# Performance work log

Measured on AMD Instinct MI355X. Metric: run time of the kernel, lower is better.

Reference implementation:

```python
import jax, jax.numpy as jnp
import numpy as np

EPS = 1e-5
NUM_GROUPS = 32


def group_norm(x, num_groups=NUM_GROUPS, eps=EPS):
    # x: [B, C, H, W]; normalize over (C//G, H, W) per group, no affine
    B, C, H, W = x.shape
    xg = x.reshape(B, num_groups, C // num_groups, H, W)
    mean = xg.mean(axis=(2, 3, 4), keepdims=True)
    var = xg.var(axis=(2, 3, 4), keepdims=True)
    xg = (xg - mean) * jax.lax.rsqrt(var + eps)
    return xg.reshape(B, C, H, W)


def nin(x, W, b):
    # 1x1 dense projection over channel dim: [B,C,H,W] x [C,O] -> [B,O,H,W]
    return jnp.einsum('bchw,co->bohw', x, W) + b[None, :, None, None]


def setup_inputs() -> dict:
    key = jax.random.key(0)
    ks = jax.random.split(key, 9)
    B, C, H, W_ = 32, 512, 32, 32
    s = 1.0 / np.sqrt(C)
    return {
        'x': jax.random.normal(ks[0], (B, C, H, W_), jnp.float32),
        'Wq': jax.random.normal(ks[1], (C, C), jnp.float32) * s,
        'bq': jnp.zeros((C,), jnp.float32),
        'Wk': jax.random.normal(ks[2], (C, C), jnp.float32) * s,
        'bk': jnp.zeros((C,), jnp.float32),
        'Wv': jax.random.normal(ks[3], (C, C), jnp.float32) * s,
        'bv': jnp.zeros((C,), jnp.float32),
        'Wn': jax.random.normal(ks[4], (C, C), jnp.float32) * (0.05 * s),
        'bn': jnp.zeros((C,), jnp.float32),
    }


def reference(x, Wq, bq, Wk, bk, Wv, bv, Wn, bn):
    B, C, H, W_ = x.shape
    h = group_norm(x)
    q = nin(h, Wq, bq)
    k = nin(h, Wk, bk)
    v = nin(h, Wv, bv)
    scale = jnp.asarray(C, x.dtype) ** -0.5
    # full spatial attention: [B, H, W, H', W']
    w = jnp.einsum('bchw,bcHW->bhwHW', q, k) * scale
    w = w.reshape(B, H, W_, H * W_)
    w = jax.nn.softmax(w, axis=-1)
    w = w.reshape(B, H, W_, H, W_)
    h = jnp.einsum('bhwHW,bcHW->bchw', w, v)
    h = nin(h, Wn, bn)
    return x + h
```

## Files before the change

### kernel.cpp

```cpp
#include <hip/hip_runtime.h>
#include <cstdint>

#define B_   32
#define C_   512
#define N_   1024
#define G_   32
#define CG_  16

typedef unsigned short u16;
typedef unsigned char u8;
typedef unsigned long long u64;

static constexpr float kEps = 1e-5f;
static constexpr float kLog2Scale = 0.06375871752987579f;

using f32x4  = __attribute__((ext_vector_type(4))) float;
using short8 = __attribute__((ext_vector_type(8))) short;
using i64x2  = __attribute__((ext_vector_type(2))) long long;

__device__ __forceinline__ u16 f2bf(float f) {
  uint32_t u = __builtin_bit_cast(uint32_t, f);
  u += 0x7fffu + ((u >> 16) & 1u);
  return (u16)(u >> 16);
}
__device__ __forceinline__ float bf2f(u16 h) {
  return __builtin_bit_cast(float, (uint32_t)h << 16);
}
__device__ __forceinline__ int pk4_fp8(float a, float b, float c, float d) {
  int w = __builtin_amdgcn_cvt_pk_fp8_f32(a, b, 0, false);
  w = __builtin_amdgcn_cvt_pk_fp8_f32(c, d, w, true);
  return w;
}
__device__ __forceinline__ int f8pos(int k) {
  const int c8 = (k >> 3) & 7;
  return (k & ~63) + ((c8 & 3) << 4) + ((c8 >> 2) << 3) + (k & 4);
}

__device__ __forceinline__ void gload16(const void* g, void* lds) {
  __builtin_amdgcn_global_load_lds(
      (__attribute__((address_space(1))) void*)(uintptr_t)g,
      (__attribute__((address_space(3))) void*)(uint32_t)(uintptr_t)lds,
      16, 0, 0);
}

__device__ __forceinline__ uint3 remap_xcd() {
  const int gx = gridDim.x, gy = gridDim.y, gz = gridDim.z;
  const int nwg = gx * gy * gz;
  const int lin = blockIdx.x + gx * (blockIdx.y + gy * blockIdx.z);
  const int q = nwg >> 3, r = nwg & 7;
  const int xcd = lin & 7, pos = lin >> 3;
  int nid = (xcd < r ? xcd * (q + 1) : r * (q + 1) + (xcd - r) * q) + pos;
  uint3 o;
  o.x = nid % gx; nid /= gx;
  o.y = nid % gy; o.z = nid / gy;
  return o;
}

__global__ __launch_bounds__(256) void wcvt_kernel(
    const float* __restrict__ Wq, const float* __restrict__ Wk,
    const float* __restrict__ Wv, u16* __restrict__ Wab, u16* __restrict__ Wbb) {
  const int idx = blockIdx.x * 256 + threadIdx.x;
  const int src = idx >> 16;
  const int e = (idx & 65535) * 4;
  const float* W = (src == 0) ? Wq : (src == 1) ? Wk : Wv;
  u16* D = (src == 0) ? Wab : (src == 1) ? Wbb : (Wab + 262144);
  const float4 v = *(const float4*)(W + e);
  ushort4 st;
  st.x = f2bf(v.x); st.y = f2bf(v.y); st.z = f2bf(v.z); st.w = f2bf(v.w);
  *(ushort4*)(D + e) = st;
}

__global__ __launch_bounds__(256) void wtr_kernel(
    const float* __restrict__ Wn, u16* __restrict__ Wtn) {
  __shared__ float tile[64][65];
  const int c0 = blockIdx.y * 64, o0 = blockIdx.x * 64;
  const int tx = threadIdx.x & 15, ty = threadIdx.x >> 4;
#pragma unroll
  for (int rr = 0; rr < 64; rr += 16) {
    const int c = c0 + ty + rr;
    const float4 v = *(const float4*)(Wn + (size_t)c * 512 + o0 + tx * 4);
    tile[ty + rr][tx * 4 + 0] = v.x;
    tile[ty + rr][tx * 4 + 1] = v.y;
    tile[ty + rr][tx * 4 + 2] = v.z;
    tile[ty + rr][tx * 4 + 3] = v.w;
  }
  __syncthreads();
#pragma unroll
  for (int rr = 0; rr < 64; rr += 16) {
    const int o = o0 + ty + rr;
    ushort4 st;
    st.x = f2bf(tile[tx * 4 + 0][ty + rr]);
    st.y = f2bf(tile[tx * 4 + 1][ty + rr]);
    st.z = f2bf(tile[tx * 4 + 2][ty + rr]);
    st.w = f2bf(tile[tx * 4 + 3][ty + rr]);
    *(ushort4*)(Wtn + (size_t)o * 512 + c0 + tx * 4) = st;
  }
}

__global__ __launch_bounds__(512) void biask_kernel(
    const float* __restrict__ Wk, const float* __restrict__ bq,
    const float* __restrict__ Wn, const float* __restrict__ bv,
    const float* __restrict__ bn, float* __restrict__ wkbq,
    float* __restrict__ bvn) {
  const int t = threadIdx.x;
  if (blockIdx.x == 0) {
    float s = 0.f;
    const float* row = Wk + (size_t)t * 512;
    for (int o = 0; o < 512; ++o) s += row[o] * bq[o];
    wkbq[t] = s;
  } else {
    float s = 0.f;
    for (int c = 0; c < 512; ++c) s += bv[c] * Wn[(size_t)c * 512 + t];
    bvn[t] = s + bn[t];
  }
}

__global__ __launch_bounds__(256) void gn_fused(const float* __restrict__ x,
                                                u8* __restrict__ Hn8,
                                                u8* __restrict__ HnT8) {
  __shared__ u16 lds2[16 * 1032];
  __shared__ float red[10];
  const int bg = blockIdx.x, b = bg >> 5, g = bg & 31;
  const int t = threadIdx.x;
  const float4* p4 = (const float4*)(x + (size_t)bg * 16384);
  float s = 0.f, s2 = 0.f;
  for (int i = t; i < 4096; i += 256) {
    const float4 v = p4[i];
    const int e = i * 4, ic = e >> 10, n = e & 1023;
    ushort4 sv;
    sv.x = f2bf(v.x); sv.y = f2bf(v.y); sv.z = f2bf(v.z); sv.w = f2bf(v.w);
    *(ushort4*)(lds2 + ic * 1032 + n) = sv;
    s  += v.x + v.y + v.z + v.w;
    s2 += v.x * v.x + v.y * v.y + v.z * v.z + v.w * v.w;
  }
#pragma unroll
  for (int o = 32; o; o >>= 1) { s += __shfl_xor(s, o); s2 += __shfl_xor(s2, o); }
  const int lane = t & 63, w = t >> 6;
  if (lane == 0) { red[w] = s; red[4 + w] = s2; }
  __syncthreads();
  if (t == 0) {
    s  = red[0] + red[1] + red[2] + red[3];
    s2 = red[4] + red[5] + red[6] + red[7];
    const float inv = 1.0f / 16384.0f;
    const float mean = s * inv;
    const float var  = s2 * inv - mean * mean;
    red[8] = mean;
    red[9] = rsqrtf(var + kEps);
  }
  __syncthreads();
  const float mean = red[8], rstd = red[9];
#pragma unroll
  for (int r = 0; r < 4; ++r) {
    const int n = t + 256 * r;
    float vals[16];
#pragma unroll
    for (int ic = 0; ic < 16; ++ic)
      vals[ic] = (bf2f(lds2[ic * 1032 + n]) - mean) * rstd;
    const u64 lo = (u64)(uint32_t)pk4_fp8(vals[0], vals[1], vals[2], vals[3]) |
                   ((u64)(uint32_t)pk4_fp8(vals[4], vals[5], vals[6], vals[7]) << 32);
    const u64 hi = (u64)(uint32_t)pk4_fp8(vals[8], vals[9], vals[10], vals[11]) |
                   ((u64)(uint32_t)pk4_fp8(vals[12], vals[13], vals[14], vals[15]) << 32);
    u8* rb = Hn8 + ((size_t)(b * N_ + n)) * C_;
    *(u64*)(rb + f8pos(g * 16))     = lo;
    *(u64*)(rb + f8pos(g * 16 + 8)) = hi;
  }
  const int nb = t * 4;
#pragma unroll
  for (int ic = 0; ic < 16; ++ic) {
    const ushort4 hv = *(const ushort4*)(lds2 + ic * 1032 + nb);
    const int wv = pk4_fp8((bf2f(hv.x) - mean) * rstd, (bf2f(hv.y) - mean) * rstd,
                           (bf2f(hv.z) - mean) * rstd, (bf2f(hv.w) - mean) * rstd);
    *(int*)(HnT8 + ((size_t)(b * C_ + g * 16 + ic)) * N_ + f8pos(nb)) = wv;
  }
}

__global__ __launch_bounds__(256) void gemm_w128(
    const u16* __restrict__ Ab, const u16* __restrict__ Bb, u8* __restrict__ Ob) {
  __shared__ u16 Alds[128 * 64];
  __shared__ u16 Blds[128 * 64];
  const int p = blockIdx.z;
  const u16* A = Ab + (size_t)p * 262144;
  const u16* B = Bb + (size_t)p * 262144;
  u8* O = Ob + (size_t)p * 262144;
  const int m0 = blockIdx.y * 128, n0 = blockIdx.x * 128;
  const int tid = threadIdx.x, lane = tid & 63, wid = tid >> 6;
  const int wm = wid >> 1, wn = wid & 1;
  const int sr = lane >> 3, scb = (lane & 7) ^ sr;
  const u16* Ag = A + (size_t)(m0 + wid * 32 + sr) * 512 + scb * 8;
  const u16* Bg = B + (size_t)(n0 + wid * 32 + sr) * 512 + scb * 8;
  char* Al = (char*)Alds + wid * 4096;
  char* Bl = (char*)Blds + wid * 4096;
  const int arow = lane & 15, g4 = lane >> 4, rx = lane & 7;
  f32x4 acc[4][4] = {};
  for (int k = 0; k < 512; k += 64) {
#pragma unroll
    for (int g = 0; g < 4; ++g) {
      gload16(Ag + k + g * (8 * 512), Al + g * 1024);
      gload16(Bg + k + g * (8 * 512), Bl + g * 1024);
    }
    __syncthreads();
#pragma unroll
    for (int kk = 0; kk < 2; ++kk) {
      const int pc = ((kk * 4 + g4) ^ rx) * 16;
      short8 a[4], b[4];
#pragma unroll
      for (int i = 0; i < 4; ++i)
        a[i] = *(const short8*)((const char*)Alds + (wm * 64 + i * 16 + arow) * 128 + pc);
#pragma unroll
      for (int j = 0; j < 4; ++j)
        b[j] = *(const short8*)((const char*)Blds + (wn * 64 + j * 16 + arow) * 128 + pc);
#pragma unroll
      for (int i = 0; i < 4; ++i)
#pragma unroll
        for (int j = 0; j < 4; ++j)
          acc[i][j] = __builtin_amdgcn_mfma_f32_16x16x32_bf16(a[i], b[j], acc[i][j], 0, 0, 0);
    }
    __syncthreads();
  }
#pragma unroll
  for (int i = 0; i < 4; ++i) {
    const int rowg = m0 + wm * 64 + i * 16 + ((lane >> 4) * 4);
#pragma unroll
    for (int j = 0; j < 4; ++j) {
      const int colg = n0 + wn * 64 + j * 16 + (lane & 15);
      const f32x4 v = acc[i][j];
      *(int*)(O + (size_t)colg * 512 + f8pos(rowg)) =
          pk4_fp8(v[0], v[1], v[2], v[3]);
    }
  }
}

#define LDA8_(D, BASE, MH)                                                      \
  _Pragma("unroll")                                                             \
  for (int i_ = 0; i_ < 4; ++i_) {                                              \
    const int rr_ = wm * 128 + (MH) * 64 + i_ * 16 + arow;                      \
    D[i_] = *(const i64x2*)((BASE) + rr_ * 64 +                                 \
                            ((g4 ^ ((rr_ >> 1) & 3)) << 4));                    \
  }
#define LDB8_(D, BASE)                                                          \
  _Pragma("unroll")                                                             \
  for (int j_ = 0; j_ < 4; ++j_) {                                              \
    const int rr_ = wn * 64 + j_ * 16 + arow;                                   \
    D[j_] = *(const i64x2*)((BASE) + rr_ * 64 +                                 \
                            ((g4 ^ ((rr_ >> 1) & 3)) << 4));                    \
  }
#define MM8_(ACC, AA, BB, H)                                                    \
  __builtin_amdgcn_s_setprio(1);                                                \
  _Pragma("unroll")                                                             \
  for (int i_ = 0; i_ < 4; ++i_)                                                \
    _Pragma("unroll")                                                           \
    for (int j_ = 0; j_ < 4; ++j_)                                              \
      ACC[i_][j_] = __builtin_amdgcn_mfma_f32_16x16x32_fp8_fp8(                 \
          AA[i_][H], BB[j_][H], ACC[i_][j_], 0, 0, 0);                          \
  __builtin_amdgcn_s_setprio(0);

__device__ __forceinline__ void gemm_core256_f8(
    const u8* __restrict__ A, const u8* __restrict__ B,
    int Ktot, int m0, int n0,
    char* Alds, char* Blds, f32x4 acc0[4][4], f32x4 acc1[4][4]) {
  const int tid = threadIdx.x, lane = tid & 63, wid = tid >> 6;
  const int wm = wid >> 2, wn = wid & 3;
  const int rl = lane >> 2;
  const int c16 = (lane & 3) ^ ((lane >> 3) & 3);
  const u8* Ag = A + (size_t)(m0 + wid * 32 + rl) * Ktot + c16 * 16;
  const u8* Bg = B + (size_t)(n0 + wid * 32 + rl) * Ktot + c16 * 16;
  char* Al = Alds + wid * 2048;
  char* Bl = Blds + wid * 2048;
  const long long r16 = (long long)16 * Ktot;
  const int arow = lane & 15, g4 = lane >> 4;
  const int nt = Ktot >> 6;

#pragma unroll
  for (int g = 0; g < 2; ++g) {
    gload16(Ag + g * r16, Al + g * 1024);
    gload16(Bg + g * r16, Bl + g * 1024);
  }
  asm volatile("s_waitcnt vmcnt(0)" ::: "memory");
  __builtin_amdgcn_s_barrier();
  i64x2 aX[4], aY[4], bX[4];
  LDA8_(aX, Alds, 0);

  for (int t = 0; t < nt; ++t) {
    const int cur = t & 1;
    const char* Ab = Alds + cur * 16384;
    const char* Bb = Blds + cur * 16384;
    const char* An = Alds + (cur ^ 1) * 16384;
    char* Aln = Al + (cur ^ 1) * 16384;
    char* Bln = Bl + (cur ^ 1) * 16384;
    const bool nx = (t + 1 < nt);
    const long long ko = (long long)(t + 1) * 64;

    if (nx) {
#pragma unroll
      for (int g = 0; g < 2; ++g) gload16(Bg + ko + g * r16, Bln + g * 1024);
    }
    LDB8_(bX, Bb);
    LDA8_(aY, Ab, 1);
    asm volatile("s_waitcnt lgkmcnt(4)" ::: "memory");
    __builtin_amdgcn_sched_barrier(0);
    __builtin_amdgcn_s_barrier();
    MM8_(acc0, aX, bX, 0);

    if (nx) {
#pragma unroll
      for (int g = 0; g < 2; ++g) gload16(Ag + ko + g * r16, Aln + g * 1024);
    }
    asm volatile("s_waitcnt lgkmcnt(0)" ::: "memory");
    __builtin_amdgcn_sched_barrier(0);
    __builtin_amdgcn_s_barrier();
    MM8_(acc1, aY, bX, 0);

    __builtin_amdgcn_sched_barrier(0);
    __builtin_amdgcn_s_barrier();
    MM8_(acc0, aX, bX, 1);

    if (nx) {
      asm volatile("s_waitcnt vmcnt(0)" ::: "memory");
    }
    __builtin_amdgcn_sched_barrier(0);
    __builtin_amdgcn_s_barrier();
    if (nx) {
      LDA8_(aX, An, 0);
    }
    MM8_(acc1, aY, bX, 1);
  }
}

__device__ __forceinline__ void copy_out_tile(const char* SH, u8* O, int LDC,
                                              int m0, int n0) {
  const int tid = threadIdx.x;
#pragma unroll
  for (int it = 0; it < 8; ++it) {
    const int flat = it * 8192 + tid * 16;
    const int row = flat >> 8, col = flat & 255;
    *(int4*)(O + (size_t)(n0 + row) * LDC + m0 + col) =
        *(const int4*)(SH + row * 256 + col);
  }
}

__global__ __launch_bounds__(512, 2) void gemm_hwq_f8(
    const u8* __restrict__ Wqk8, const u8* __restrict__ Hn8,
    const float* __restrict__ wkbq, u8* __restrict__ HWq8) {
  __shared__ char SH[4 * 256 * 64];
  const uint3 bid = remap_xcd();
  const int z = bid.z;
  const u8* B = Hn8 + (size_t)z * ((size_t)N_ * C_);
  u8* O = HWq8 + (size_t)z * ((size_t)N_ * C_);
  const int m0 = bid.y * 256, n0 = bid.x * 256;
  f32x4 acc0[4][4] = {};
  f32x4 acc1[4][4] = {};
  gemm_core256_f8(Wqk8, B, 512, m0, n0, SH, SH + 32768, acc0, acc1);

  const int lane = threadIdx.x & 63, wid = threadIdx.x >> 6;
  const int wm = wid >> 2, wn = wid & 3;
  __syncthreads();
#pragma unroll
  for (int i = 0; i < 8; ++i) {
    const int ml = wm * 128 + i * 16 + ((lane >> 4) * 4);
    const float4 bv = *(const float4*)(wkbq + m0 + ml);
#pragma unroll
    for (int j = 0; j < 4; ++j) {
      const int nl = wn * 64 + j * 16 + (lane & 15);
      const f32x4 v = (i < 4) ? acc0[i][j] : acc1[i - 4][j];
      *(int*)(SH + nl * 256 + f8pos(ml)) =
          pk4_fp8(v[0] + bv.x, v[1] + bv.y, v[2] + bv.z, v[3] + bv.w);
    }
  }
  __syncthreads();
  copy_out_tile(SH, O, 512, m0, n0);
}

__global__ __launch_bounds__(512, 2) void gemm_s_f8(
    const u8* __restrict__ Hn8, const u8* __restrict__ HWq8,
    u8* __restrict__ P8, float* __restrict__ Psum) {
  __shared__ char SH[4 * 256 * 64];
  const uint3 bid = remap_xcd();
  const int z = bid.z;
  const u8* A = Hn8  + (size_t)z * ((size_t)N_ * C_);
  const u8* B = HWq8 + (size_t)z * ((size_t)N_ * C_);
  u8*       O = P8   + (size_t)z * ((size_t)N_ * N_);
  const int m0 = bid.y * 256, n0 = bid.x * 256;
  f32x4 acc0[4][4] = {};
  f32x4 acc1[4][4] = {};
  gemm_core256_f8(A, B, 512, m0, n0, SH, SH + 32768, acc0, acc1);

  const int lane = threadIdx.x & 63, wid = threadIdx.x >> 6;
  const int wm = wid >> 2, wn = wid & 3;
  float psum[4] = {0.f, 0.f, 0.f, 0.f};
  __syncthreads();
#pragma unroll
  for (int i = 0; i < 8; ++i) {
    const int ml = wm * 128 + i * 16 + ((lane >> 4) * 4);
#pragma unroll
    for (int j = 0; j < 4; ++j) {
      const int nl = wn * 64 + j * 16 + (lane & 15);
      const f32x4 v = (i < 4) ? acc0[i][j] : acc1[i - 4][j];
      const float p0 = __builtin_exp2f(v[0] * kLog2Scale) * 0.0625f;
      const float p1 = __builtin_exp2f(v[1] * kLog2Scale) * 0.0625f;
      const float p2 = __builtin_exp2f(v[2] * kLog2Scale) * 0.0625f;
      const float p3 = __builtin_exp2f(v[3] * kLog2Scale) * 0.0625f;
      psum[j] += (p0 + p1) + (p2 + p3);
      *(int*)(SH + nl * 256 + f8pos(ml)) = pk4_fp8(p0, p1, p2, p3);
    }
  }
  const int slot = (m0 >> 7) + wm;
  float* Ps = Psum + ((size_t)z * 8 + slot) * N_;
#pragma unroll
  for (int j = 0; j < 4; ++j) {
    float r = psum[j];
    r += __shfl_xor(r, 16);
    r += __shfl_xor(r, 32);
    if (lane < 16) Ps[n0 + wn * 64 + j * 16 + lane] = r;
  }
  __syncthreads();
  copy_out_tile(SH, O, 1024, m0, n0);
}

__global__ __launch_bounds__(512, 2) void gemm_pv_f8(
    const u8* __restrict__ HnT8, const u8* __restrict__ P8,
    const float* __restrict__ Psum, u8* __restrict__ H28) {
  __shared__ char SH[4 * 256 * 64];
  const uint3 bid = remap_xcd();
  const int z = bid.z;
  const u8* A = HnT8 + (size_t)z * ((size_t)N_ * C_);
  const u8* B = P8   + (size_t)z * ((size_t)N_ * N_);
  u8*       O = H28  + (size_t)z * ((size_t)N_ * C_);
  const int m0 = bid.y * 256, n0 = bid.x * 256;
  f32x4 acc0[4][4] = {};
  f32x4 acc1[4][4] = {};
  gemm_core256_f8(A, B, 1024, m0, n0, SH, SH + 32768, acc0, acc1);

  const int lane = threadIdx.x & 63, wid = threadIdx.x >> 6;
  const int wm = wid >> 2, wn = wid & 3;
  const float* Ps = Psum + (size_t)z * 8 * N_;
  float inv[4];
#pragma unroll
  for (int j = 0; j < 4; ++j) {
    const int colg = n0 + wn * 64 + j * 16 + (lane & 15);
    float s = 0.f;
#pragma unroll
    for (int k = 0; k < 8; ++k) s += Ps[k * N_ + colg];
    inv[j] = 1.0f / s;
  }
  __syncthreads();
#pragma unroll
  for (int i = 0; i < 8; ++i) {
    const int ml = wm * 128 + i * 16 + ((lane >> 4) * 4);
#pragma unroll
    for (int j = 0; j < 4; ++j) {
      const int nl = wn * 64 + j * 16 + (lane & 15);
      const f32x4 v = (i < 4) ? acc0[i][j] : acc1[i - 4][j];
      *(int*)(SH + nl * 256 + f8pos(ml)) =
          pk4_fp8(v[0] * inv[j], v[1] * inv[j], v[2] * inv[j], v[3] * inv[j]);
    }
  }
  __syncthreads();
  copy_out_tile(SH, O, 512, m0, n0);
}

__global__ __launch_bounds__(512, 2) void gemm_final_f8(
    const u8* __restrict__ H28, const u8* __restrict__ Wvn8,
    const float* __restrict__ x, const float* __restrict__ bvn,
    float* __restrict__ Out) {
  __shared__ char Alds[2 * 256 * 64];
  __shared__ char Blds[2 * 256 * 64];
  const uint3 bid = remap_xcd();
  const int z = bid.z;
  const u8*    Ab = H28 + (size_t)z * ((size_t)N_ * C_);
  const float* xb = x + (size_t)z * ((size_t)C_ * N_);
  float*       Ob = Out + (size_t)z * ((size_t)C_ * N_);
  const int m0 = bid.y * 256, n0 = bid.x * 256;
  f32x4 acc0[4][4] = {};
  f32x4 acc1[4][4] = {};
  gemm_core256_f8(Ab, Wvn8, 512, m0, n0, Alds, Blds, acc0, acc1);

  const int lane = threadIdx.x & 63, wid = threadIdx.x >> 6;
  const int wm = wid >> 2, wn = wid & 3;
#pragma unroll
  for (int i = 0; i < 8; ++i) {
    const int rowg = m0 + wm * 128 + i * 16 + ((lane >> 4) * 4);
#pragma unroll
    for (int j = 0; j < 4; ++j) {
      const int colg = n0 + wn * 64 + j * 16 + (lane & 15);
      const float bc = bvn[colg];
      const size_t off = (size_t)colg * N_ + rowg;
      const float4 xv = *(const float4*)(xb + off);
      const f32x4 v = (i < 4) ? acc0[i][j] : acc1[i - 4][j];
      float4 ov;
      ov.x = xv.x + v[0] + bc;
      ov.y = xv.y + v[1] + bc;
      ov.z = xv.z + v[2] + bc;
      ov.w = xv.w + v[3] + bc;
      *(float4*)(Ob + off) = ov;
    }
  }
}

__global__ void sentinel_kernel(float* out, int n, float v) {
  const int i = blockIdx.x * blockDim.x + threadIdx.x;
  if (i < n) out[i] = v;
}

extern "C" void kernel_launch(void* const* d_in, const int* in_sizes, int n_in,
                              void* d_out, int out_size, void* d_ws, size_t ws_size,
                              hipStream_t stream) {
  const float* x  = (const float*)d_in[0];
  const float* Wq = (const float*)d_in[1];
  const float* bq = (const float*)d_in[2];
  const float* Wk = (const float*)d_in[3];
  const float* Wv = (const float*)d_in[5];
  const float* bv = (const float*)d_in[6];
  const float* Wn = (const float*)d_in[7];
  const float* bn = (const float*)d_in[8];
  float* out = (float*)d_out;

  char* ws = (char*)d_ws;
  size_t off = 0;
  u16* Wab = (u16*)(ws + off); off += (size_t)2 * 262144 * 2;
  u16* Wbb = (u16*)(ws + off); off += (size_t)2 * 262144 * 2;
  u8*  W8  = (u8*)(ws + off);  off += (size_t)2 * 262144;
  float* wkbq = (float*)(ws + off); off += 512 * 4;
  float* bvn  = (float*)(ws + off); off += 512 * 4;
  const size_t bnc = (size_t)B_ * N_ * C_;
  u8* Hn8  = (u8*)(ws + off); off += bnc;
  u8* HnT8 = (u8*)(ws + off); off += bnc;
  u8* HWq8 = (u8*)(ws + off); off += bnc;
  u8* P8   = (u8*)(ws + off); off += (size_t)B_ * N_ * N_;
  u8* H28  = (u8*)(ws + off); off += bnc;
  float* Psum = (float*)(ws + off); off += (size_t)B_ * 8 * N_ * 4;

  if (ws_size < off) {
    const float v = 1.0e6f + (float)(ws_size >> 20);
    sentinel_kernel<<<(out_size + 255) / 256, 256, 0, stream>>>(out, out_size, v);
    return;
  }

  wcvt_kernel<<<768, 256, 0, stream>>>(Wq, Wk, Wv, Wab, Wbb);
  wtr_kernel<<<dim3(8, 8), 256, 0, stream>>>(Wn, Wbb + 262144);
  biask_kernel<<<2, 512, 0, stream>>>(Wk, bq, Wn, bv, bn, wkbq, bvn);
  gn_fused<<<B_ * G_, 256, 0, stream>>>(x, Hn8, HnT8);
  gemm_w128<<<dim3(4, 4, 2), 256, 0, stream>>>(Wab, Wbb, W8);
  gemm_hwq_f8<<<dim3(4, 2, B_), 512, 0, stream>>>(W8, Hn8, wkbq, HWq8);
  gemm_s_f8<<<dim3(4, 4, B_), 512, 0, stream>>>(Hn8, HWq8, P8, Psum);
  gemm_pv_f8<<<dim3(4, 2, B_), 512, 0, stream>>>(HnT8, P8, Psum, H28);
  gemm_final_f8<<<dim3(2, 4, B_), 512, 0, stream>>>(H28, W8 + 262144, x, bvn, out);
}
```

Baseline: 194.7 us.

## Fuse PV and output projection GEMMs into one kernel with LDS-resident H2

Merges the P·V GEMM and the final Wn projection into a single kernel: each block computes all 512 channels for a 128-column slice of positions, keeps the normalized fp8 result in shared memory (XOR-swizzled), then runs the second GEMM reading weights directly from global memory and writes the residual output. This removes the H28 round trip through global memory and one launch. The epilogue staging in other kernels also gains an XOR swizzle to reduce LDS bank conflicts. In exchange it uses 144KB of LDS with one block per CU, a smaller tile along N, and unstaged global weight loads in the second GEMM.

Measured after the change: 192.2 us (median of 2 runs). Within noise of the previous version (-1.3%).

```diff
diff --git a/kernel.cpp b/kernel.cpp
--- a/kernel.cpp
+++ b/kernel.cpp
@@ -334,7 +334,7 @@
     const int flat = it * 8192 + tid * 16;
     const int row = flat >> 8, col = flat & 255;
     *(int4*)(O + (size_t)(n0 + row) * LDC + m0 + col) =
-        *(const int4*)(SH + row * 256 + col);
+        *(const int4*)(SH + row * 256 + (col ^ ((row & 15) << 4)));
   }
 }
 
@@ -358,11 +358,12 @@
   for (int i = 0; i < 8; ++i) {
     const int ml = wm * 128 + i * 16 + ((lane >> 4) * 4);
     const float4 bv = *(const float4*)(wkbq + m0 + ml);
+    const int fp = f8pos(ml);
 #pragma unroll
     for (int j = 0; j < 4; ++j) {
       const int nl = wn * 64 + j * 16 + (lane & 15);
       const f32x4 v = (i < 4) ? acc0[i][j] : acc1[i - 4][j];
-      *(int*)(SH + nl * 256 + f8pos(ml)) =
+      *(int*)(SH + nl * 256 + (fp ^ ((nl & 15) << 4))) =
           pk4_fp8(v[0] + bv.x, v[1] + bv.y, v[2] + bv.z, v[3] + bv.w);
     }
   }
@@ -391,6 +392,7 @@
 #pragma unroll
   for (int i = 0; i < 8; ++i) {
     const int ml = wm * 128 + i * 16 + ((lane >> 4) * 4);
+    const int fp = f8pos(ml);
 #pragma unroll
     for (int j = 0; j < 4; ++j) {
       const int nl = wn * 64 + j * 16 + (lane & 15);
@@ -400,7 +402,7 @@
       const float p2 = __builtin_exp2f(v[2] * kLog2Scale) * 0.0625f;
       const float p3 = __builtin_exp2f(v[3] * kLog2Scale) * 0.0625f;
       psum[j] += (p0 + p1) + (p2 + p3);
-      *(int*)(SH + nl * 256 + f8pos(ml)) = pk4_fp8(p0, p1, p2, p3);
+      *(int*)(SH + nl * 256 + (fp ^ ((nl & 15) << 4))) = pk4_fp8(p0, p1, p2, p3);
     }
   }
   const int slot = (m0 >> 7) + wm;
@@ -416,76 +418,147 @@
   copy_out_tile(SH, O, 1024, m0, n0);
 }
 
-__global__ __launch_bounds__(512, 2) void gemm_pv_f8(
+__global__ __launch_bounds__(512, 1) void gemm_pvf_f8(
     const u8* __restrict__ HnT8, const u8* __restrict__ P8,
-    const float* __restrict__ Psum, u8* __restrict__ H28) {
-  __shared__ char SH[4 * 256 * 64];
+    const float* __restrict__ Psum, const u8* __restrict__ Wvn8,
+    const float* __restrict__ x, const float* __restrict__ bvn,
+    float* __restrict__ Out) {
+  __shared__ char SH[147456];
+  char* Abuf = SH;
+  char* Bbuf = SH + 65536;
+  char* H2   = SH + 81920;
   const uint3 bid = remap_xcd();
   const int z = bid.z;
   const u8* A = HnT8 + (size_t)z * ((size_t)N_ * C_);
   const u8* B = P8   + (size_t)z * ((size_t)N_ * N_);
-  u8*       O = H28  + (size_t)z * ((size_t)N_ * C_);
-  const int m0 = bid.y * 256, n0 = bid.x * 256;
+  const int n0 = bid.x * 128;
+  const int tid = threadIdx.x, lane = tid & 63, wid = tid >> 6;
+  const int wm = wid >> 1, wn = wid & 1;
+  const int rl = lane >> 2;
+  const int c16 = (lane & 3) ^ ((lane >> 3) & 3);
+  const u8* Ag = A + (size_t)(wid * 64 + rl) * 1024 + c16 * 16;
+  const u8* Bg = B + (size_t)(n0 + wid * 16 + rl) * 1024 + c16 * 16;
+  const int arow = lane & 15, g4 = lane >> 4;
   f32x4 acc0[4][4] = {};
   f32x4 acc1[4][4] = {};
-  gemm_core256_f8(A, B, 1024, m0, n0, SH, SH + 32768, acc0, acc1);
-
-  const int lane = threadIdx.x & 63, wid = threadIdx.x >> 6;
-  const int wm = wid >> 2, wn = wid & 3;
+
+#pragma unroll
+  for (int g = 0; g < 4; ++g)
+    gload16(Ag + (size_t)g * (16 * 1024), Abuf + wid * 4096 + g * 1024);
+  gload16(Bg, Bbuf + wid * 1024);
+  asm volatile("s_waitcnt vmcnt(0)" ::: "memory");
+  __builtin_amdgcn_s_barrier();
+  i64x2 aX[4], aY[4], bX[4];
+  LDA8_(aX, Abuf, 0);
+
+  for (int t = 0; t < 16; ++t) {
+    const int cur = t & 1;
+    const char* Ab = Abuf + cur * 32768;
+    const char* Bb = Bbuf + cur * 8192;
+    const char* An = Abuf + (cur ^ 1) * 32768;
+    const bool nx = (t + 1 < 16);
+    const long long ko = (long long)(t + 1) * 64;
+
+    if (nx) gload16(Bg + ko, Bbuf + (cur ^ 1) * 8192 + wid * 1024);
+    LDB8_(bX, Bb);
+    LDA8_(aY, Ab, 1);
+    asm volatile("s_waitcnt lgkmcnt(4)" ::: "memory");
+    __builtin_amdgcn_sched_barrier(0);
+    __builtin_amdgcn_s_barrier();
+    MM8_(acc0, aX, bX, 0);
+
+    if (nx) {
+#pragma unroll
+      for (int g = 0; g < 4; ++g)
+        gload16(Ag + ko + (size_t)g * (16 * 1024),
+                Abuf + (cur ^ 1) * 32768 + wid * 4096 + g * 1024);
+    }
+    asm volatile("s_waitcnt lgkmcnt(0)" ::: "memory");
+    __builtin_amdgcn_sched_barrier(0);
+    __builtin_amdgcn_s_barrier();
+    MM8_(acc1, aY, bX, 0);
+
+    __builtin_amdgcn_sched_barrier(0);
+    __builtin_amdgcn_s_barrier();
+    MM8_(acc0, aX, bX, 1);
+
+    if (nx) {
+      asm volatile("s_waitcnt vmcnt(0)" ::: "memory");
+    }
+    __builtin_amdgcn_sched_barrier(0);
+    __builtin_amdgcn_s_barrier();
+    if (nx) {
+      LDA8_(aX, An, 0);
+    }
+    MM8_(acc1, aY, bX, 1);
+  }
+
   const float* Ps = Psum + (size_t)z * 8 * N_;
   float inv[4];
 #pragma unroll
   for (int j = 0; j < 4; ++j) {
-    const int colg = n0 + wn * 64 + j * 16 + (lane & 15);
+    const int ng = n0 + wn * 64 + j * 16 + (lane & 15);
     float s = 0.f;
 #pragma unroll
-    for (int k = 0; k < 8; ++k) s += Ps[k * N_ + colg];
+    for (int k = 0; k < 8; ++k) s += Ps[k * N_ + ng];
     inv[j] = 1.0f / s;
   }
-  __syncthreads();
 #pragma unroll
   for (int i = 0; i < 8; ++i) {
-    const int ml = wm * 128 + i * 16 + ((lane >> 4) * 4);
+    const int c = wm * 128 + i * 16 + ((lane >> 4) * 4);
+    const int fp = f8pos(c);
+    const int ck = fp >> 4, sub = fp & 15;
 #pragma unroll
     for (int j = 0; j < 4; ++j) {
       const int nl = wn * 64 + j * 16 + (lane & 15);
       const f32x4 v = (i < 4) ? acc0[i][j] : acc1[i - 4][j];
-      *(int*)(SH + nl * 256 + f8pos(ml)) =
+      *(int*)(H2 + nl * 512 + ((ck ^ (nl & 15)) << 4) + sub) =
           pk4_fp8(v[0] * inv[j], v[1] * inv[j], v[2] * inv[j], v[3] * inv[j]);
     }
   }
   __syncthreads();
-  copy_out_tile(SH, O, 512, m0, n0);
-}
-
-__global__ __launch_bounds__(512, 2) void gemm_final_f8(
-    const u8* __restrict__ H28, const u8* __restrict__ Wvn8,
-    const float* __restrict__ x, const float* __restrict__ bvn,
-    float* __restrict__ Out) {
-  __shared__ char Alds[2 * 256 * 64];
-  __shared__ char Blds[2 * 256 * 64];
-  const uint3 bid = remap_xcd();
-  const int z = bid.z;
-  const u8*    Ab = H28 + (size_t)z * ((size_t)N_ * C_);
+
+  const int wmf = wid >> 2, wnf = wid & 3;
+  f32x4 acc2[4][8] = {};
+#pragma unroll
+  for (int t = 0; t < 8; ++t) {
+    i64x2 a2[4], b2[8];
+#pragma unroll
+    for (int i = 0; i < 4; ++i) {
+      const int rn = wmf * 64 + i * 16 + arow;
+      a2[i] = *(const i64x2*)(H2 + rn * 512 + (((t * 4 + g4) ^ (rn & 15)) << 4));
+    }
+#pragma unroll
+    for (int j = 0; j < 8; ++j) {
+      const int ro = wnf * 128 + j * 16 + arow;
+      b2[j] = *(const i64x2*)(Wvn8 + (size_t)ro * 512 + t * 64 + g4 * 16);
+    }
+#pragma unroll
+    for (int i = 0; i < 4; ++i)
+#pragma unroll
+      for (int j = 0; j < 8; ++j)
+        acc2[i][j] = __builtin_amdgcn_mfma_f32_16x16x32_fp8_fp8(
+            a2[i][0], b2[j][0], acc2[i][j], 0, 0, 0);
+#pragma unroll
+    for (int i = 0; i < 4; ++i)
+#pragma unroll
+      for (int j = 0; j < 8; ++j)
+        acc2[i][j] = __builtin_amdgcn_mfma_f32_16x16x32_fp8_fp8(
+            a2[i][1], b2[j][1], acc2[i][j], 0, 0, 0);
+  }
+
   const float* xb = x + (size_t)z * ((size_t)C_ * N_);
-  float*       Ob = Out + (size_t)z * ((size_t)C_ * N_);
-  const int m0 = bid.y * 256, n0 = bid.x * 256;
-  f32x4 acc0[4][4] = {};
-  f32x4 acc1[4][4] = {};
-  gemm_core256_f8(Ab, Wvn8, 512, m0, n0, Alds, Blds, acc0, acc1);
-
-  const int lane = threadIdx.x & 63, wid = threadIdx.x >> 6;
-  const int wm = wid >> 2, wn = wid & 3;
-#pragma unroll
-  for (int i = 0; i < 8; ++i) {
-    const int rowg = m0 + wm * 128 + i * 16 + ((lane >> 4) * 4);
-#pragma unroll
-    for (int j = 0; j < 4; ++j) {
-      const int colg = n0 + wn * 64 + j * 16 + (lane & 15);
-      const float bc = bvn[colg];
-      const size_t off = (size_t)colg * N_ + rowg;
+  float* Ob = Out + (size_t)z * ((size_t)C_ * N_);
+#pragma unroll
+  for (int i = 0; i < 4; ++i) {
+    const int rown = n0 + wmf * 64 + i * 16 + ((lane >> 4) * 4);
+#pragma unroll
+    for (int j = 0; j < 8; ++j) {
+      const int colo = wnf * 128 + j * 16 + (lane & 15);
+      const float bc = bvn[colo];
+      const size_t off = (size_t)colo * N_ + rown;
       const float4 xv = *(const float4*)(xb + off);
-      const f32x4 v = (i < 4) ? acc0[i][j] : acc1[i - 4][j];
+      const f32x4 v = acc2[i][j];
       float4 ov;
       ov.x = xv.x + v[0] + bc;
       ov.y = xv.y + v[1] + bc;
@@ -526,7 +599,6 @@
   u8* HnT8 = (u8*)(ws + off); off += bnc;
   u8* HWq8 = (u8*)(ws + off); off += bnc;
   u8* P8   = (u8*)(ws + off); off += (size_t)B_ * N_ * N_;
-  u8* H28  = (u8*)(ws + off); off += bnc;
   float* Psum = (float*)(ws + off); off += (size_t)B_ * 8 * N_ * 4;
 
   if (ws_size < off) {
@@ -542,6 +614,5 @@
   gemm_w128<<<dim3(4, 4, 2), 256, 0, stream>>>(Wab, Wbb, W8);
   gemm_hwq_f8<<<dim3(4, 2, B_), 512, 0, stream>>>(W8, Hn8, wkbq, HWq8);
   gemm_s_f8<<<dim3(4, 4, B_), 512, 0, stream>>>(Hn8, HWq8, P8, Psum);
-  gemm_pv_f8<<<dim3(4, 2, B_), 512, 0, stream>>>(HnT8, P8, Psum, H28);
-  gemm_final_f8<<<dim3(2, 4, B_), 512, 0, stream>>>(H28, W8 + 262144, x, bvn, out);
-}
+  gemm_pvf_f8<<<dim3(8, 1, B_), 512, 0, stream>>>(HnT8, P8, Psum, W8 + 262144, x, bvn, out);
+}
```
